# Kernel tuning notes

Measured on AMD Instinct MI355X. Metric: run time of the kernel, lower is better.

Reference implementation:

```python
import jax, jax.numpy as jnp
import numpy as np

NUM_GEMMS = 64      # local experts (num_gemms)
IN_SIZE = 2048      # input_size == config.hidden_size (column parallel)
OUT_SIZE = 1408     # per-expert output width
TOTAL_TOKENS = 32768


def setup_inputs() -> dict:
    key = jax.random.key(0)
    kx, kw = jax.random.split(key)
    x = jax.random.normal(kx, (TOTAL_TOKENS, IN_SIZE), dtype=jnp.float32)
    # torch params are [output_size, input_size] per expert -> stack to [E, out, in]
    W = jax.random.normal(kw, (NUM_GEMMS, OUT_SIZE, IN_SIZE), dtype=jnp.float32) * 0.02
    # uneven per-expert row splits, sum == TOTAL_TOKENS (avg 512, alternating 256/768)
    m_splits = jnp.array([256, 768] * (NUM_GEMMS // 2), dtype=jnp.int32)
    return {"x": x, "W": W, "m_splits": m_splits}


def reference(x, W, m_splits):
    # original: original_weight = cat([w.t() for w in weights]) -> [E*in, out]
    # column mode: view(E, hidden, -1) -> [E, in, out]; gmm over row splits.
    w = jnp.transpose(W, (0, 2, 1))  # [E, in, out]
    splits = np.asarray(m_splits)    # row splits are static metadata of the grouped GEMM
    offs = np.concatenate([[0], np.cumsum(splits)])
    # grouped GEMM: out[rows_of_e] = x[rows_of_e] @ w[e]; loop is over the fixed expert set
    outs = [x[offs[e]:offs[e + 1]] @ w[e] for e in range(w.shape[0])]
    return jnp.concatenate(outs, axis=0)  # [total_tokens, out]
```

## Files before the change

kernel.cpp:

```cpp
#include <hip/hip_runtime.h>
#include <hip/hip_bf16.h>

#define E_ 64
#define K_ 2048
#define N_ 1408
#define BM 256
#define BN 128
#define BK 32
#define NK (K_ / BK)
#define NTHREADS 512
#define NTILE (N_ / BN)
#define LDSA (BM * BK * 2)
#define LDSB (BN * BK * 2)
#define LDSBUF (LDSA + LDSB)
#define GRID_ 2112

using f32x4  = __attribute__((ext_vector_type(4))) float;
using bf16x8 = __attribute__((ext_vector_type(8))) short;

#define BAR() asm volatile("s_waitcnt lgkmcnt(0)\n\ts_barrier" ::: "memory")

__device__ __forceinline__ short f2b(float f) {
  __hip_bfloat16 h = __float2bfloat16(f);
  return __builtin_bit_cast(short, h);
}

__global__ void build_meta(const int* __restrict__ m_splits, int* __restrict__ meta) {
  const int e = threadIdx.x;
  const int m = m_splits[e];
  const int mt = (m + BM - 1) / BM;
  int sm = m, smt = mt;
#pragma unroll
  for (int d = 1; d < 64; d <<= 1) {
    const int vm = __shfl_up(sm, d);
    const int vt = __shfl_up(smt, d);
    if (e >= d) { sm += vm; smt += vt; }
  }
  meta[1 + e] = smt - mt;
  meta[66 + e] = sm - m;
  if (e == 63) { meta[1 + 64] = smt; meta[0] = smt * NTILE; }
}

struct Stage { f32x4 a[2][2]; f32x4 b[2]; };

__global__ __launch_bounds__(NTHREADS, 2) void gemm_grouped(
    const float* __restrict__ x, const float* __restrict__ W,
    const int* __restrict__ m_splits, const int* __restrict__ meta,
    float* __restrict__ out) {
  __shared__ char smem[2 * LDSBUF];

  const int J = meta[0];
  const int xcd = blockIdx.x & 7;
  const int pos = blockIdx.x >> 3;
  const int q = J >> 3, r = J & 7;
  if (pos >= q + (xcd < r ? 1 : 0)) return;
  const int jidx = xcd * q + min(xcd, r) + pos;

  int lo = 0, hi = 64;
  while (hi - lo > 1) {
    const int mid = (lo + hi) >> 1;
    if (meta[1 + mid] * NTILE <= jidx) lo = mid; else hi = mid;
  }
  const int e = lo;
  const int mt_e = meta[1 + e + 1] - meta[1 + e];
  const int rem = jidx - meta[1 + e] * NTILE;
  const int nt = rem / mt_e;
  const int t  = rem - nt * mt_e;
  const int m_e = m_splits[e];
  const int row0 = meta[66 + e] + t * BM;
  const int nrows = min(BM, m_e - t * BM);
  const int n0 = nt * BN;

  const int tid  = threadIdx.x;
  const int lane = tid & 63;
  const int w    = tid >> 6;
  const int wm   = w >> 1;
  const int wn   = w & 1;

  const int strow = tid >> 2;
  const int skc8  = (tid & 3) * 8;
  const int kcb   = (tid & 3) * 16;

  const float* xrow = x + (size_t)row0 * K_;
  const float* wrow = W + ((size_t)e * N_ + (size_t)n0) * K_;
  const f32x4 zero4 = {0.f, 0.f, 0.f, 0.f};

  auto load_tiles = [&](int kt, Stage& st) {
    const int kbase = kt * BK + skc8;
#pragma unroll
    for (int c = 0; c < 2; ++c) {
      const int rr = c * 128 + strow;
      if (rr < nrows) {
        const float* pp = xrow + (size_t)rr * K_ + kbase;
        st.a[c][0] = *(const f32x4*)pp;
        st.a[c][1] = *(const f32x4*)(pp + 4);
      } else { st.a[c][0] = zero4; st.a[c][1] = zero4; }
    }
    const float* qq = wrow + (size_t)strow * K_ + kbase;
    st.b[0] = *(const f32x4*)qq;
    st.b[1] = *(const f32x4*)(qq + 4);
  };

  auto write_lds = [&](int buf, const Stage& st) {
    const int base = buf * LDSBUF;
#pragma unroll
    for (int c = 0; c < 2; ++c) {
      const int rr = c * 128 + strow;
      const int off = rr * 64 + (kcb ^ (((rr >> 1) & 3) << 4));
      bf16x8 v;
#pragma unroll
      for (int i = 0; i < 4; ++i) { v[i] = f2b(st.a[c][0][i]); v[i + 4] = f2b(st.a[c][1][i]); }
      *(bf16x8*)(smem + base + off) = v;
    }
    {
      const int rr = strow;
      const int off = rr * 64 + (kcb ^ (((rr >> 1) & 3) << 4));
      bf16x8 v;
#pragma unroll
      for (int i = 0; i < 4; ++i) { v[i] = f2b(st.b[0][i]); v[i + 4] = f2b(st.b[1][i]); }
      *(bf16x8*)(smem + base + LDSA + off) = v;
    }
  };

  f32x4 acc[4][4];
#pragma unroll
  for (int i = 0; i < 4; ++i)
#pragma unroll
    for (int j = 0; j < 4; ++j) acc[i][j] = zero4;

  const int arow0 = wm * 64 + (lane & 15);
  const int brow0 = wn * 64 + (lane & 15);
  const int kslot = (lane >> 4) * 16;

  auto compute = [&](int buf) {
    const int base = buf * LDSBUF;
    bf16x8 af[4], bfr[4];
#pragma unroll
    for (int i = 0; i < 4; ++i) {
      const int rr = arow0 + i * 16;
      af[i] = *(const bf16x8*)(smem + base + rr * 64 + (kslot ^ (((rr >> 1) & 3) << 4)));
    }
#pragma unroll
    for (int j = 0; j < 4; ++j) {
      const int rr = brow0 + j * 16;
      bfr[j] = *(const bf16x8*)(smem + base + LDSA + rr * 64 + (kslot ^ (((rr >> 1) & 3) << 4)));
    }
    __builtin_amdgcn_s_setprio(1);
#pragma unroll
    for (int i = 0; i < 4; ++i)
#pragma unroll
      for (int j = 0; j < 4; ++j)
        acc[i][j] = __builtin_amdgcn_mfma_f32_16x16x32_bf16(af[i], bfr[j], acc[i][j], 0, 0, 0);
    __builtin_amdgcn_s_setprio(0);
  };

  Stage sA;
  load_tiles(0, sA);
  write_lds(0, sA);
  int cur = 0;
  for (int kt = 0; kt < NK; ++kt) {
    if (kt + 1 < NK) load_tiles(kt + 1, sA);
    BAR();
    compute(cur);
    if (kt + 1 < NK) write_lds(cur ^ 1, sA);
    cur ^= 1;
  }

  const int crow = wm * 64 + (lane >> 4) * 4;
  const int ccol = n0 + wn * 64 + (lane & 15);
#pragma unroll
  for (int i = 0; i < 4; ++i) {
#pragma unroll
    for (int rr = 0; rr < 4; ++rr) {
      const int lr = crow + i * 16 + rr;
      if (lr < nrows) {
#pragma unroll
        for (int j = 0; j < 4; ++j)
          out[(size_t)(row0 + lr) * N_ + ccol + j * 16] = acc[i][j][rr];
      }
    }
  }
}

extern "C" void kernel_launch(void* const* d_in, const int* in_sizes, int n_in,
                              void* d_out, int out_size, void* d_ws, size_t ws_size,
                              hipStream_t stream) {
  const float* x        = (const float*)d_in[0];
  const float* W        = (const float*)d_in[1];
  const int*   m_splits = (const int*)d_in[2];
  float*       out      = (float*)d_out;

  int* meta = (int*)d_ws;

  build_meta<<<1, 64, 0, stream>>>(m_splits, meta);
  gemm_grouped<<<GRID_, NTHREADS, 0, stream>>>(x, W, m_splits, meta, out);
}
```

Before: 406.4 us.

## Double K-tile depth and interleave global loads with MFMA phases

Doubles the K tile from 32 to 64, which halves the number of main-loop iterations, and uses a 128-byte LDS row with an XOR swizzle over 8 slots. Each iteration is split into four MFMA phases separated by barriers, and the global loads for the next tile (B, then two halves of A) are issued between those phases. The intent is to overlap memory latency with compute and cut per-iteration barrier overhead. The costs are more barriers inside each iteration, more registers held for staged fp32 data, and double the LDS footprint, which could affect occupancy at 2 blocks per CU.

```diff
diff --git a/kernel.cpp b/kernel.cpp
--- a/kernel.cpp
+++ b/kernel.cpp
@@ -6,13 +6,13 @@
 #define N_ 1408
 #define BM 256
 #define BN 128
-#define BK 32
-#define NK (K_ / BK)
+#define BK 64
+#define NT (K_ / BK)
 #define NTHREADS 512
 #define NTILE (N_ / BN)
-#define LDSA (BM * BK * 2)
-#define LDSB (BN * BK * 2)
-#define LDSBUF (LDSA + LDSB)
+#define LDSA_B (BM * BK * 2)
+#define LDSB_B (BN * BK * 2)
+#define LDSBUF (LDSA_B + LDSB_B)
 #define GRID_ 2112
 
 using f32x4  = __attribute__((ext_vector_type(4))) float;
@@ -40,8 +40,6 @@
   meta[66 + e] = sm - m;
   if (e == 63) { meta[1 + 64] = smt; meta[0] = smt * NTILE; }
 }
-
-struct Stage { f32x4 a[2][2]; f32x4 b[2]; };
 
 __global__ __launch_bounds__(NTHREADS, 2) void gemm_grouped(
     const float* __restrict__ x, const float* __restrict__ W,
@@ -65,10 +63,10 @@
   const int mt_e = meta[1 + e + 1] - meta[1 + e];
   const int rem = jidx - meta[1 + e] * NTILE;
   const int nt = rem / mt_e;
-  const int t  = rem - nt * mt_e;
+  const int t_  = rem - nt * mt_e;
   const int m_e = m_splits[e];
-  const int row0 = meta[66 + e] + t * BM;
-  const int nrows = min(BM, m_e - t * BM);
+  const int row0 = meta[66 + e] + t_ * BM;
+  const int nrows = min(BM, m_e - t_ * BM);
   const int n0 = nt * BN;
 
   const int tid  = threadIdx.x;
@@ -77,94 +75,129 @@
   const int wm   = w >> 1;
   const int wn   = w & 1;
 
-  const int strow = tid >> 2;
-  const int skc8  = (tid & 3) * 8;
-  const int kcb   = (tid & 3) * 16;
+  const int arow_s = tid >> 1;
+  const int acol_s = (tid & 1) * 32;
+  const int brow_s = tid >> 2;
+  const int bcol_s = (tid & 3) * 16;
 
   const float* xrow = x + (size_t)row0 * K_;
   const float* wrow = W + ((size_t)e * N_ + (size_t)n0) * K_;
   const f32x4 zero4 = {0.f, 0.f, 0.f, 0.f};
 
-  auto load_tiles = [&](int kt, Stage& st) {
-    const int kbase = kt * BK + skc8;
+  f32x4 sa[8], sb[4];
+
+  auto load_B = [&](int kt) {
+    const float* p = wrow + (size_t)brow_s * K_ + kt * BK + bcol_s;
+#pragma unroll
+    for (int c = 0; c < 4; ++c) sb[c] = *(const f32x4*)(p + c * 4);
+  };
+  auto load_A0 = [&](int kt) {
+    if (arow_s < nrows) {
+      const float* p = xrow + (size_t)arow_s * K_ + kt * BK + acol_s;
+#pragma unroll
+      for (int c = 0; c < 4; ++c) sa[c] = *(const f32x4*)(p + c * 4);
+    } else {
+#pragma unroll
+      for (int c = 0; c < 4; ++c) sa[c] = zero4;
+    }
+  };
+  auto load_A1 = [&](int kt) {
+    if (arow_s < nrows) {
+      const float* p = xrow + (size_t)arow_s * K_ + kt * BK + acol_s + 16;
+#pragma unroll
+      for (int c = 0; c < 4; ++c) sa[4 + c] = *(const f32x4*)(p + c * 4);
+    } else {
+#pragma unroll
+      for (int c = 0; c < 4; ++c) sa[4 + c] = zero4;
+    }
+  };
+
+  auto write_AB = [&](int buf) {
+    const int ab = buf * LDSBUF;
+#pragma unroll
+    for (int c = 0; c < 4; ++c) {
+      const int slot = (((tid & 1) * 4 + c)) ^ (arow_s & 7);
+      bf16x8 v;
+#pragma unroll
+      for (int i = 0; i < 4; ++i) { v[i] = f2b(sa[2 * c][i]); v[i + 4] = f2b(sa[2 * c + 1][i]); }
+      *(bf16x8*)(smem + ab + arow_s * 128 + slot * 16) = v;
+    }
 #pragma unroll
     for (int c = 0; c < 2; ++c) {
-      const int rr = c * 128 + strow;
-      if (rr < nrows) {
-        const float* pp = xrow + (size_t)rr * K_ + kbase;
-        st.a[c][0] = *(const f32x4*)pp;
-        st.a[c][1] = *(const f32x4*)(pp + 4);
-      } else { st.a[c][0] = zero4; st.a[c][1] = zero4; }
-    }
-    const float* qq = wrow + (size_t)strow * K_ + kbase;
-    st.b[0] = *(const f32x4*)qq;
-    st.b[1] = *(const f32x4*)(qq + 4);
-  };
-
-  auto write_lds = [&](int buf, const Stage& st) {
-    const int base = buf * LDSBUF;
-#pragma unroll
-    for (int c = 0; c < 2; ++c) {
-      const int rr = c * 128 + strow;
-      const int off = rr * 64 + (kcb ^ (((rr >> 1) & 3) << 4));
+      const int slot = (((tid & 3) * 2 + c)) ^ (brow_s & 7);
       bf16x8 v;
 #pragma unroll
-      for (int i = 0; i < 4; ++i) { v[i] = f2b(st.a[c][0][i]); v[i + 4] = f2b(st.a[c][1][i]); }
-      *(bf16x8*)(smem + base + off) = v;
-    }
-    {
-      const int rr = strow;
-      const int off = rr * 64 + (kcb ^ (((rr >> 1) & 3) << 4));
-      bf16x8 v;
-#pragma unroll
-      for (int i = 0; i < 4; ++i) { v[i] = f2b(st.b[0][i]); v[i + 4] = f2b(st.b[1][i]); }
-      *(bf16x8*)(smem + base + LDSA + off) = v;
-    }
-  };
-
-  f32x4 acc[4][4];
-#pragma unroll
-  for (int i = 0; i < 4; ++i)
-#pragma unroll
-    for (int j = 0; j < 4; ++j) acc[i][j] = zero4;
+      for (int i = 0; i < 4; ++i) { v[i] = f2b(sb[2 * c][i]); v[i + 4] = f2b(sb[2 * c + 1][i]); }
+      *(bf16x8*)(smem + ab + LDSA_B + brow_s * 128 + slot * 16) = v;
+    }
+  };
 
   const int arow0 = wm * 64 + (lane & 15);
   const int brow0 = wn * 64 + (lane & 15);
-  const int kslot = (lane >> 4) * 16;
-
-  auto compute = [&](int buf) {
-    const int base = buf * LDSBUF;
-    bf16x8 af[4], bfr[4];
-#pragma unroll
-    for (int i = 0; i < 4; ++i) {
-      const int rr = arow0 + i * 16;
-      af[i] = *(const bf16x8*)(smem + base + rr * 64 + (kslot ^ (((rr >> 1) & 3) << 4)));
-    }
-#pragma unroll
-    for (int j = 0; j < 4; ++j) {
-      const int rr = brow0 + j * 16;
-      bfr[j] = *(const bf16x8*)(smem + base + LDSA + rr * 64 + (kslot ^ (((rr >> 1) & 3) << 4)));
-    }
-    __builtin_amdgcn_s_setprio(1);
-#pragma unroll
-    for (int i = 0; i < 4; ++i)
-#pragma unroll
-      for (int j = 0; j < 4; ++j)
-        acc[i][j] = __builtin_amdgcn_mfma_f32_16x16x32_bf16(af[i], bfr[j], acc[i][j], 0, 0, 0);
-    __builtin_amdgcn_s_setprio(0);
-  };
-
-  Stage sA;
-  load_tiles(0, sA);
-  write_lds(0, sA);
+  const int kgrp  = lane >> 4;
+
+  auto rdA = [&](int buf, int kk, int i) -> bf16x8 {
+    const int row = arow0 + i * 16;
+    const int slot = (kk * 4 + kgrp) ^ (row & 7);
+    return *(const bf16x8*)(smem + buf * LDSBUF + row * 128 + slot * 16);
+  };
+  auto rdB = [&](int buf, int kk, int j) -> bf16x8 {
+    const int row = brow0 + j * 16;
+    const int slot = (kk * 4 + kgrp) ^ (row & 7);
+    return *(const bf16x8*)(smem + buf * LDSBUF + LDSA_B + row * 128 + slot * 16);
+  };
+
+  f32x4 acc[4][4];
+#pragma unroll
+  for (int i = 0; i < 4; ++i)
+#pragma unroll
+    for (int j = 0; j < 4; ++j) acc[i][j] = zero4;
+
+#define MFMA8(J0, J1)                                                         \
+  __builtin_amdgcn_s_setprio(1);                                              \
+  acc[0][J0] = __builtin_amdgcn_mfma_f32_16x16x32_bf16(fa0, fb0, acc[0][J0], 0, 0, 0); \
+  acc[1][J0] = __builtin_amdgcn_mfma_f32_16x16x32_bf16(fa1, fb0, acc[1][J0], 0, 0, 0); \
+  acc[2][J0] = __builtin_amdgcn_mfma_f32_16x16x32_bf16(fa2, fb0, acc[2][J0], 0, 0, 0); \
+  acc[3][J0] = __builtin_amdgcn_mfma_f32_16x16x32_bf16(fa3, fb0, acc[3][J0], 0, 0, 0); \
+  acc[0][J1] = __builtin_amdgcn_mfma_f32_16x16x32_bf16(fa0, fb1, acc[0][J1], 0, 0, 0); \
+  acc[1][J1] = __builtin_amdgcn_mfma_f32_16x16x32_bf16(fa1, fb1, acc[1][J1], 0, 0, 0); \
+  acc[2][J1] = __builtin_amdgcn_mfma_f32_16x16x32_bf16(fa2, fb1, acc[2][J1], 0, 0, 0); \
+  acc[3][J1] = __builtin_amdgcn_mfma_f32_16x16x32_bf16(fa3, fb1, acc[3][J1], 0, 0, 0); \
+  __builtin_amdgcn_s_setprio(0);
+
+  load_B(0); load_A0(0); load_A1(0);
+  write_AB(0);
+  BAR();
+
   int cur = 0;
-  for (int kt = 0; kt < NK; ++kt) {
-    if (kt + 1 < NK) load_tiles(kt + 1, sA);
-    BAR();
-    compute(cur);
-    if (kt + 1 < NK) write_lds(cur ^ 1, sA);
-    cur ^= 1;
-  }
+  for (int t = 0; t < NT; ++t) {
+    const bool hn = (t + 1 < NT);
+    const int nxt = cur ^ 1;
+    bf16x8 fa0, fa1, fa2, fa3, fb0, fb1;
+    fa0 = rdA(cur, 0, 0); fa1 = rdA(cur, 0, 1); fa2 = rdA(cur, 0, 2); fa3 = rdA(cur, 0, 3);
+    fb0 = rdB(cur, 0, 0); fb1 = rdB(cur, 0, 1);
+    if (hn) load_B(t + 1);
+    BAR();
+    MFMA8(0, 1)
+    fb0 = rdB(cur, 0, 2); fb1 = rdB(cur, 0, 3);
+    if (hn) load_A0(t + 1);
+    BAR();
+    MFMA8(2, 3)
+    fa0 = rdA(cur, 1, 0); fa1 = rdA(cur, 1, 1); fa2 = rdA(cur, 1, 2); fa3 = rdA(cur, 1, 3);
+    fb0 = rdB(cur, 1, 0); fb1 = rdB(cur, 1, 1);
+    if (hn) load_A1(t + 1);
+    BAR();
+    MFMA8(0, 1)
+    fb0 = rdB(cur, 1, 2); fb1 = rdB(cur, 1, 3);
+    BAR();
+    MFMA8(2, 3)
+    if (hn) {
+      write_AB(nxt);
+      BAR();
+    }
+    cur = nxt;
+  }
+#undef MFMA8
 
   const int crow = wm * 64 + (lane >> 4) * 4;
   const int ccol = n0 + wn * 64 + (lane & 15);
```

Result: slower. 666.3 us (+64.0%).
